# Kernel tuning notes

Measured on AMD Instinct MI355X. Metric: run time of the kernel, lower is better.

Reference implementation:

```python
import jax, jax.numpy as jnp
import numpy as np

CH = 512      # channels
CI = CH // 4  # in_channel = 128
DILS = (1, 4, 8, 12)
GN_GROUPS = 32


def conv2d(x, w, dil=1, pad=0):
    # x: (N,Cin,H,W), w: (Cout,Cin,kh,kw)
    return jax.lax.conv_general_dilated(
        x, w, window_strides=(1, 1), padding=[(pad, pad), (pad, pad)],
        rhs_dilation=(dil, dil),
        dimension_numbers=('NCHW', 'OIHW', 'NCHW'))


def group_norm(x, gamma, beta, groups=GN_GROUPS, eps=1e-5):
    N, C, H, W = x.shape
    xg = x.reshape(N, groups, C // groups, H, W)
    mu = jnp.mean(xg, axis=(2, 3, 4), keepdims=True)
    var = jnp.var(xg, axis=(2, 3, 4), keepdims=True)
    xn = ((xg - mu) * jax.lax.rsqrt(var + eps)).reshape(N, C, H, W)
    return xn * gamma[None, :, None, None] + beta[None, :, None, None]


def dyn_branch(xd, w_cat, d):
    # dynamic filter: (N, 9, H, W), softmax over the K=9 taps per pixel
    f = jax.nn.softmax(conv2d(xd, w_cat, dil=d, pad=d), axis=1)
    N, C, H, W = xd.shape
    xp = jnp.pad(xd, ((0, 0), (0, 0), (d, d), (d, d)))
    # fused unfold + weighted sum: accumulate 9 shifted views * per-pixel weight
    out = jnp.zeros_like(xd)
    k = 0
    for i in range(3):
        for j in range(3):
            out = out + xp[:, :, i * d:i * d + H, j * d:j * d + W] * f[:, k:k + 1]
            k += 1
    return out


def setup_inputs():
    key = jax.random.key(0)
    ks = jax.random.split(key, 16)
    s = 0.05
    return {
        'x': jax.random.normal(ks[0], (4, CH, 128, 128), jnp.float32),
        'w_scale1': jax.random.normal(ks[1], (CI, CH, 1, 1), jnp.float32) * s,
        'gn1_g': jnp.ones((CI,), jnp.float32),
        'gn1_b': jnp.zeros((CI,), jnp.float32),
        'w_cata': jax.random.normal(ks[2], (9, CI, 3, 3), jnp.float32) * s,
        'w_catb': jax.random.normal(ks[3], (9, CI, 3, 3), jnp.float32) * s,
        'w_catc': jax.random.normal(ks[4], (9, CI, 3, 3), jnp.float32) * s,
        'w_catd': jax.random.normal(ks[5], (9, CI, 3, 3), jnp.float32) * s,
        'w_scale2': jax.random.normal(ks[6], (CI, 5 * CI, 1, 1), jnp.float32) * s,
        'gn2_g': jnp.ones((CI,), jnp.float32),
        'gn2_b': jnp.zeros((CI,), jnp.float32),
        'w_scale3': jax.random.normal(ks[7], (CH, CI, 1, 1), jnp.float32) * s,
        'gn3_g': jnp.ones((CH,), jnp.float32),
        'gn3_b': jnp.zeros((CH,), jnp.float32),
    }


def reference(x, w_scale1, gn1_g, gn1_b, w_cata, w_catb, w_catc, w_catd,
              w_scale2, gn2_g, gn2_b, w_scale3, gn3_g, gn3_b):
    # scale1: 1x1 conv -> GN -> ReLU
    xd = jax.nn.relu(group_norm(conv2d(x, w_scale1), gn1_g, gn1_b))
    # four dilated dynamic-filter branches (unfold + softmax-weighted reduce)
    outs = [dyn_branch(xd, w, d)
            for w, d in zip((w_cata, w_catb, w_catc, w_catd), DILS)]
    cat = jnp.concatenate([xd] + outs, axis=1)  # (N, 5*CI, H, W)
    y = jax.nn.relu(group_norm(conv2d(cat, w_scale2), gn2_g, gn2_b))
    y = jax.nn.relu(group_norm(conv2d(y, w_scale3), gn3_g, gn3_b))
    return y
```

## Files before the change

kernel.cpp:

```cpp
#include <hip/hip_runtime.h>
#include <math.h>

#define HW 16384

typedef float f32x4 __attribute__((ext_vector_type(4)));
typedef __bf16 bf16x8 __attribute__((ext_vector_type(8)));
typedef unsigned short u16x4 __attribute__((ext_vector_type(4)));
typedef unsigned short u16x8 __attribute__((ext_vector_type(8)));

__device__ __forceinline__ unsigned short f2bf(float f) {
  unsigned u = __float_as_uint(f);
  u += 0x7fffu + ((u >> 16) & 1u);
  return (unsigned short)(u >> 16);
}
__device__ __forceinline__ float bf2f(unsigned short s) {
  return __uint_as_float(((unsigned)s) << 16);
}

__global__ void prep_kernel(const float* __restrict__ w1, const float* __restrict__ w2,
                            const float* __restrict__ w3,
                            const float* __restrict__ wa, const float* __restrict__ wb,
                            const float* __restrict__ wc, const float* __restrict__ wd,
                            unsigned short* __restrict__ w1b, unsigned short* __restrict__ w2b,
                            unsigned short* __restrict__ w3b, unsigned short* __restrict__ wr) {
  int idx = blockIdx.x * 256 + threadIdx.x;
  if (idx < 65536) { w1b[idx] = f2bf(w1[idx]); }
  else if (idx < 147456) { int j = idx - 65536; w2b[j] = f2bf(w2[j]); }
  else if (idx < 212992) { int j = idx - 147456; w3b[j] = f2bf(w3[j]); }
  else if (idx < 286720) {
    int j = idx - 212992;
    int br = j / 18432, rem = j % 18432;
    int tap = rem / 2048, rem2 = rem % 2048;
    int kt = rem2 / 128, c = rem2 % 128;
    const float* w = (br == 0) ? wa : (br == 1) ? wb : (br == 2) ? wc : wd;
    float v = (kt < 9) ? w[(kt * 128 + c) * 9 + tap] : 0.f;
    wr[j] = f2bf(v);
  }
}

__global__ __launch_bounds__(256) void conv1f_kernel(
    const float* __restrict__ x, const unsigned short* __restrict__ w1b,
    float* __restrict__ out) {
  __shared__ float xs[2][64][65];
  int t = threadIdx.x;
  int wv = t >> 6, lane = t & 63, lr = lane & 15, lg = lane >> 4;
  int n = blockIdx.y;
  int p0 = blockIdx.x * 64;
  const float* xn = x + (size_t)n * 512 * HW + p0;
  f32x4 acc[8];
#pragma unroll
  for (int cb = 0; cb < 8; ++cb) acc[cb] = (f32x4){0.f, 0.f, 0.f, 0.f};

  int ci_l = t >> 4, px4 = (t & 15) * 4;
  float4 r[4];

#pragma unroll
  for (int pass = 0; pass < 4; ++pass)
    r[pass] = *(const float4*)(xn + (size_t)(pass * 16 + ci_l) * HW + px4);
#pragma unroll
  for (int pass = 0; pass < 4; ++pass) {
    int cl = pass * 16 + ci_l;
    xs[0][cl][px4 + 0] = r[pass].x; xs[0][cl][px4 + 1] = r[pass].y;
    xs[0][cl][px4 + 2] = r[pass].z; xs[0][cl][px4 + 3] = r[pass].w;
  }

  for (int kt = 0; kt < 8; ++kt) {
    int cur = kt & 1;
    if (kt < 7) {
#pragma unroll
      for (int pass = 0; pass < 4; ++pass)
        r[pass] = *(const float4*)(xn + (size_t)((kt + 1) * 64 + pass * 16 + ci_l) * HW + px4);
    }
    __syncthreads();
#pragma unroll
    for (int ks = 0; ks < 2; ++ks) {
      bf16x8 a;
#pragma unroll
      for (int j = 0; j < 8; ++j) {
        unsigned short us = f2bf(xs[cur][ks * 32 + lg * 8 + j][wv * 16 + lr]);
        a[j] = *(__bf16*)&us;
      }
#pragma unroll
      for (int cb = 0; cb < 8; ++cb) {
        bf16x8 b = *(const bf16x8*)(w1b + (size_t)(cb * 16 + lr) * 512
                                    + kt * 64 + ks * 32 + lg * 8);
        acc[cb] = __builtin_amdgcn_mfma_f32_16x16x32_bf16(a, b, acc[cb], 0, 0, 0);
      }
    }
    if (kt < 7) {
#pragma unroll
      for (int pass = 0; pass < 4; ++pass) {
        int cl = pass * 16 + ci_l;
        xs[cur ^ 1][cl][px4 + 0] = r[pass].x; xs[cur ^ 1][cl][px4 + 1] = r[pass].y;
        xs[cur ^ 1][cl][px4 + 2] = r[pass].z; xs[cur ^ 1][cl][px4 + 3] = r[pass].w;
      }
    }
  }
  float* on = out + (size_t)n * HW * 128;
#pragma unroll
  for (int cb = 0; cb < 8; ++cb)
#pragma unroll
    for (int r2 = 0; r2 < 4; ++r2)
      on[(size_t)(p0 + wv * 16 + lg * 4 + r2) * 128 + cb * 16 + lr] = acc[cb][r2];
}

template<int K>
__global__ __launch_bounds__(256) void conv_pm_kernel(
    const unsigned short* __restrict__ act, const unsigned short* __restrict__ w,
    float* __restrict__ out) {
  int wv = threadIdx.x >> 6, lane = threadIdx.x & 63;
  int lr = lane & 15, lg = lane >> 4;
  int n = blockIdx.y;
  int p0 = blockIdx.x * 64 + wv * 16;
  const unsigned short* an = act + (size_t)n * HW * K;
  f32x4 acc[8];
#pragma unroll
  for (int cb = 0; cb < 8; ++cb) acc[cb] = (f32x4){0.f, 0.f, 0.f, 0.f};
  const unsigned short* ap = an + (size_t)(p0 + lr) * K + lg * 8;
  const unsigned short* bp = w + (size_t)lr * K + lg * 8;
  for (int ks = 0; ks < K / 32; ++ks) {
    bf16x8 a = *(const bf16x8*)(ap + ks * 32);
#pragma unroll
    for (int cb = 0; cb < 8; ++cb) {
      bf16x8 b = *(const bf16x8*)(bp + (size_t)cb * 16 * K + ks * 32);
      acc[cb] = __builtin_amdgcn_mfma_f32_16x16x32_bf16(a, b, acc[cb], 0, 0, 0);
    }
  }
  float* on = out + (size_t)n * HW * 128;
#pragma unroll
  for (int cb = 0; cb < 8; ++cb)
#pragma unroll
    for (int r = 0; r < 4; ++r)
      on[(size_t)(p0 + lg * 4 + r) * 128 + cb * 16 + lr] = acc[cb][r];
}

__global__ __launch_bounds__(256) void conv3_kernel(
    const unsigned short* __restrict__ y, const unsigned short* __restrict__ w3,
    unsigned short* __restrict__ outb, float* __restrict__ part) {
  int wv = threadIdx.x >> 6, lane = threadIdx.x & 63;
  int lr = lane & 15, lg = lane >> 4;
  int n = blockIdx.y, zc = blockIdx.z;
  int co0 = zc * 128 + wv * 32;
  int p0 = blockIdx.x * 128;
  const unsigned short* yn = y + (size_t)n * HW * 128;
  f32x4 acc[2][8];
#pragma unroll
  for (int pr = 0; pr < 2; ++pr)
#pragma unroll
    for (int cb = 0; cb < 8; ++cb) acc[pr][cb] = (f32x4){0.f, 0.f, 0.f, 0.f};
#pragma unroll
  for (int ks = 0; ks < 4; ++ks) {
    bf16x8 a0 = *(const bf16x8*)(w3 + (size_t)(co0 + lr) * 128 + ks * 32 + lg * 8);
    bf16x8 a1 = *(const bf16x8*)(w3 + (size_t)(co0 + 16 + lr) * 128 + ks * 32 + lg * 8);
#pragma unroll
    for (int cb = 0; cb < 8; ++cb) {
      bf16x8 b = *(const bf16x8*)(yn + (size_t)(p0 + cb * 16 + lr) * 128 + ks * 32 + lg * 8);
      acc[0][cb] = __builtin_amdgcn_mfma_f32_16x16x32_bf16(a0, b, acc[0][cb], 0, 0, 0);
      acc[1][cb] = __builtin_amdgcn_mfma_f32_16x16x32_bf16(a1, b, acc[1][cb], 0, 0, 0);
    }
  }
  unsigned short* on = outb + (size_t)n * 512 * HW;
  float s[2] = {0.f, 0.f}, ss[2] = {0.f, 0.f};
#pragma unroll
  for (int pr = 0; pr < 2; ++pr)
#pragma unroll
    for (int cb = 0; cb < 8; ++cb)
#pragma unroll
      for (int r = 0; r < 4; ++r) {
        float v = acc[pr][cb][r];
        on[(size_t)(co0 + pr * 16 + lg * 4 + r) * HW + p0 + cb * 16 + lr] = f2bf(v);
        s[pr] += v; ss[pr] += v * v;
      }
#pragma unroll
  for (int pr = 0; pr < 2; ++pr) {
    float a = s[pr], b = ss[pr];
    for (int m = 1; m < 64; m <<= 1) { a += __shfl_xor(a, m); b += __shfl_xor(b, m); }
    if (lane == 0) {
      float* pp = part + ((((size_t)n * 4 + zc) * 128 + blockIdx.x) * 8 + wv * 2 + pr) * 2;
      pp[0] = a; pp[1] = b;
    }
  }
}

__global__ void gnf3_kernel(const float* __restrict__ part, float* __restrict__ stats) {
  int t = threadIdx.x;
  int n = t >> 5, g = t & 31;
  int zc = g >> 3, sub = g & 7;
  float s = 0.f, ss = 0.f;
  for (int xb = 0; xb < 128; ++xb) {
    const float* pp = part + ((((size_t)n * 4 + zc) * 128 + xb) * 8 + sub) * 2;
    s += pp[0]; ss += pp[1];
  }
  float inv = 1.f / (16.f * HW);
  float mean = s * inv, var = ss * inv - mean * mean;
  stats[2 * t] = mean; stats[2 * t + 1] = rsqrtf(var + 1e-5f);
}

__global__ __launch_bounds__(256) void gn3_apply_kernel(
    const unsigned short* __restrict__ y3b, const float* __restrict__ stats,
    const float* __restrict__ gamma, const float* __restrict__ beta,
    float* __restrict__ out) {
  size_t e8 = ((size_t)blockIdx.x * 256 + threadIdx.x) * 8;
  int n = (int)(e8 >> 23);
  int c = (int)((e8 >> 14) & 511);
  int sg = n * 32 + (c >> 4);
  float mean = stats[2 * sg], rstd = stats[2 * sg + 1];
  float scale = rstd * gamma[c];
  float shift = beta[c] - mean * scale;
  u16x8 u = *(const u16x8*)(y3b + e8);
  float4 o0, o1;
  o0.x = fmaxf(fmaf(bf2f(u[0]), scale, shift), 0.f);
  o0.y = fmaxf(fmaf(bf2f(u[1]), scale, shift), 0.f);
  o0.z = fmaxf(fmaf(bf2f(u[2]), scale, shift), 0.f);
  o0.w = fmaxf(fmaf(bf2f(u[3]), scale, shift), 0.f);
  o1.x = fmaxf(fmaf(bf2f(u[4]), scale, shift), 0.f);
  o1.y = fmaxf(fmaf(bf2f(u[5]), scale, shift), 0.f);
  o1.z = fmaxf(fmaf(bf2f(u[6]), scale, shift), 0.f);
  o1.w = fmaxf(fmaf(bf2f(u[7]), scale, shift), 0.f);
  *(float4*)(out + e8) = o0;
  *(float4*)(out + e8 + 4) = o1;
}

__global__ __launch_bounds__(256) void gnp_pm_kernel(const float* __restrict__ src,
                                                     float* __restrict__ part) {
  int t = threadIdx.x;
  int g = t & 31, ph = t >> 5;
  int pt = blockIdx.x, n = blockIdx.y;
  const float* b = src + (size_t)n * HW * 128 + 4 * g;
  float s = 0.f, ss = 0.f;
  for (int p = pt * 256 + ph; p < (pt + 1) * 256; p += 8) {
    float4 v = *(const float4*)(b + (size_t)p * 128);
    s += v.x + v.y + v.z + v.w;
    ss += v.x * v.x + v.y * v.y + v.z * v.z + v.w * v.w;
  }
  __shared__ float sh[256], sh2[256];
  sh[t] = s; sh2[t] = ss; __syncthreads();
  if (t < 128) { sh[t] += sh[t + 128]; sh2[t] += sh2[t + 128]; } __syncthreads();
  if (t < 64)  { sh[t] += sh[t + 64];  sh2[t] += sh2[t + 64];  } __syncthreads();
  if (t < 32) {
    float a = sh[t] + sh[t + 32], b2 = sh2[t] + sh2[t + 32];
    float* pp = part + ((size_t)(n * 64 + pt) * 32 + t) * 2;
    pp[0] = a; pp[1] = b2;
  }
}

__global__ void gnf_pm_kernel(const float* __restrict__ part, float* __restrict__ stats) {
  int t = threadIdx.x;
  int n = t >> 5, g = t & 31;
  float s = 0.f, ss = 0.f;
  for (int pt = 0; pt < 64; ++pt) {
    const float* pp = part + ((size_t)(n * 64 + pt) * 32 + g) * 2;
    s += pp[0]; ss += pp[1];
  }
  float inv = 1.f / (4.f * HW);
  float mean = s * inv, var = ss * inv - mean * mean;
  stats[2 * t] = mean; stats[2 * t + 1] = rsqrtf(var + 1e-5f);
}

__global__ __launch_bounds__(256) void gna_pm_kernel(
    const float* __restrict__ src, const float* __restrict__ stats,
    const float* __restrict__ gamma, const float* __restrict__ beta,
    unsigned short* __restrict__ dst, int ldd) {
  int idx = blockIdx.x * 256 + threadIdx.x;
  int g = idx & 31;
  int p = (idx >> 5) & (HW - 1);
  int n = idx >> 19;
  float4 v = *(const float4*)(src + ((size_t)n * HW + p) * 128 + 4 * g);
  int sg = n * 32 + g;
  float mean = stats[2 * sg], rstd = stats[2 * sg + 1];
  float sc0 = rstd * gamma[4 * g + 0], sc1 = rstd * gamma[4 * g + 1];
  float sc2 = rstd * gamma[4 * g + 2], sc3 = rstd * gamma[4 * g + 3];
  float sh0 = beta[4 * g + 0] - mean * sc0, sh1 = beta[4 * g + 1] - mean * sc1;
  float sh2 = beta[4 * g + 2] - mean * sc2, sh3 = beta[4 * g + 3] - mean * sc3;
  u16x4 o;
  o[0] = f2bf(fmaxf(fmaf(v.x, sc0, sh0), 0.f));
  o[1] = f2bf(fmaxf(fmaf(v.y, sc1, sh1), 0.f));
  o[2] = f2bf(fmaxf(fmaf(v.z, sc2, sh2), 0.f));
  o[3] = f2bf(fmaxf(fmaf(v.w, sc3, sh3), 0.f));
  *(u16x4*)(dst + ((size_t)n * HW + p) * ldd + 4 * g) = o;
}

#define DP 136

__global__ __launch_bounds__(512, 4) void dynfused6_kernel(
    const unsigned short* __restrict__ cat, const unsigned short* __restrict__ wr,
    unsigned short* __restrict__ catw) {
  extern __shared__ char smem[];
  unsigned short* rowbuf = (unsigned short*)smem;
  float* fl = (float*)(smem + 3 * 88 * DP * 2);
  int t = threadIdx.x;
  int bid = blockIdx.x;
  int rh = ((bid & 7) << 5) + (bid >> 3);
  int row = rh >> 1, hw = rh & 1;
  int n = blockIdx.y >> 2, br = blockIdx.y & 3;
  int d = (br == 0) ? 1 : 4 * br;
  const unsigned short* xb = cat + (size_t)n * HW * 640;

  int rg[3] = { max(row - d, 0), row, min(row + d, 127) };
  bool rv[3] = { row - d >= 0, true, row + d < 128 };
  int cbase = hw * 64 - 12;

  {
    u16x8 vreg[9];
#pragma unroll
    for (int k = 0; k < 9; ++k) {
      int ci = t + (k << 9);
      if (k == 8 && ci >= 4224) continue;
      int s = (ci >= 2816) ? 2 : (ci >= 1408 ? 1 : 0);
      int rem = ci - s * 1408;
      int slot = rem >> 4, c = rem & 15;
      int gcol = min(max(cbase + slot, 0), 127);
      vreg[k] = *(const u16x8*)(xb + ((size_t)(rg[s] * 128 + gcol)) * 640 + c * 8);
    }
#pragma unroll
    for (int k = 0; k < 9; ++k) {
      int ci = t + (k << 9);
      if (k == 8 && ci >= 4224) continue;
      int s = (ci >= 2816) ? 2 : (ci >= 1408 ? 1 : 0);
      int rem = ci - s * 1408;
      int slot = rem >> 4, c = rem & 15;
      *(u16x8*)(rowbuf + ((size_t)s * 88 + slot) * DP + c * 8) = vreg[k];
    }
  }
  __syncthreads();

  if (t < 256) {
    int wv = t >> 6, lane = t & 63;
    int lr = lane & 15, lg = lane >> 4;
    const unsigned short* wb = wr + (size_t)br * 9 * 16 * 128;
    const bf16x8 zb = {(__bf16)0.f, (__bf16)0.f, (__bf16)0.f, (__bf16)0.f,
                       (__bf16)0.f, (__bf16)0.f, (__bf16)0.f, (__bf16)0.f};
    f32x4 acc = (f32x4){0.f, 0.f, 0.f, 0.f};
    int pxl = wv * 16 + lr;
    int gw = hw * 64 + pxl;
#pragma unroll
    for (int tap = 0; tap < 9; ++tap) {
      int s = tap / 3;
      int dw = (tap % 3 - 1) * d;
      int slot = 12 + pxl + dw;
      bool val = rv[s] && ((unsigned)(gw + dw) < 128u);
      const unsigned short* ap = rowbuf + ((size_t)s * 88 + slot) * DP + lg * 8;
      const unsigned short* wt = wb + (size_t)(tap * 16 + lr) * 128 + lg * 8;
#pragma unroll
      for (int ks = 0; ks < 4; ++ks) {
        bf16x8 a = *(const bf16x8*)(ap + ks * 32);
        if (!val) a = zb;
        bf16x8 b = *(const bf16x8*)(wt + ks * 32);
        acc = __builtin_amdgcn_mfma_f32_16x16x32_bf16(a, b, acc, 0, 0, 0);
      }
    }
#pragma unroll
    for (int r = 0; r < 4; ++r) {
      float v = acc[r];
      float m = (lr < 9) ? v : -3.0e38f;
#pragma unroll
      for (int msk = 1; msk < 16; msk <<= 1) m = fmaxf(m, __shfl_xor(m, msk));
      float e = (lr < 9) ? expf(v - m) : 0.f;
      float su = e;
#pragma unroll
      for (int msk = 1; msk < 16; msk <<= 1) su += __shfl_xor(su, msk);
      fl[(wv * 16 + lg * 4 + r) * 17 + lr] = e / su;
    }
  }
  __syncthreads();

  {
    int pxl = t >> 3, c8 = t & 7;
    int gw = hw * 64 + pxl;
    float oacc[16];
#pragma unroll
    for (int i = 0; i < 16; ++i) oacc[i] = 0.f;
#pragma unroll
    for (int tap = 0; tap < 9; ++tap) {
      int s = tap / 3;
      int dw = (tap % 3 - 1) * d;
      int slot = 12 + pxl + dw;
      bool val = rv[s] && ((unsigned)(gw + dw) < 128u);
      float f = val ? fl[pxl * 17 + tap] : 0.f;
      const unsigned short* ap = rowbuf + ((size_t)s * 88 + slot) * DP + c8 * 16;
#pragma unroll
      for (int cc = 0; cc < 2; ++cc) {
        u16x8 u = *(const u16x8*)(ap + cc * 8);
#pragma unroll
        for (int i = 0; i < 8; ++i)
          oacc[cc * 8 + i] = fmaf(f, bf2f(u[i]), oacc[cc * 8 + i]);
      }
    }
    unsigned short* orow = catw + ((size_t)n * HW + row * 128 + gw) * 640
                           + 128 * (br + 1) + c8 * 16;
#pragma unroll
    for (int cc = 0; cc < 2; ++cc) {
      u16x8 o;
#pragma unroll
      for (int i = 0; i < 8; ++i) o[i] = f2bf(oacc[cc * 8 + i]);
      *(u16x8*)(orow + cc * 8) = o;
    }
  }
}

extern "C" void kernel_launch(void* const* d_in, const int* in_sizes, int n_in,
                              void* d_out, int out_size, void* d_ws, size_t ws_size,
                              hipStream_t stream) {
  const float* x   = (const float*)d_in[0];
  const float* w1  = (const float*)d_in[1];
  const float* g1  = (const float*)d_in[2];
  const float* b1  = (const float*)d_in[3];
  const float* wca = (const float*)d_in[4];
  const float* wcb = (const float*)d_in[5];
  const float* wcc = (const float*)d_in[6];
  const float* wcd = (const float*)d_in[7];
  const float* w2  = (const float*)d_in[8];
  const float* g2  = (const float*)d_in[9];
  const float* b2  = (const float*)d_in[10];
  const float* w3  = (const float*)d_in[11];
  const float* g3  = (const float*)d_in[12];
  const float* b3  = (const float*)d_in[13];
  float* out = (float*)d_out;

  float* ws = (float*)d_ws;
  float* xd_t = ws + 16777216;
  unsigned short* cat = (unsigned short*)(ws + 25165824);
  float* y2t = ws;
  unsigned short* y2b = (unsigned short*)(ws + 8388608);
  unsigned short* y3b = (unsigned short*)(ws + 25165824);
  float* aux = ws + 46137344;
  unsigned short* w1b = (unsigned short*)(aux);
  unsigned short* w2b = (unsigned short*)(aux + 32768);
  unsigned short* w3b = (unsigned short*)(aux + 73728);
  unsigned short* wr  = (unsigned short*)(aux + 106496);
  float* part  = aux + 143360;
  float* part3 = aux + 159744;
  float* st1   = aux + 192512;
  float* st2   = aux + 192768;
  float* st3   = aux + 193024;

  dim3 blk(256);
  const int dynLds = 3 * 88 * DP * 2 + 64 * 17 * 4;
  (void)hipFuncSetAttribute((const void*)dynfused6_kernel,
                            hipFuncAttributeMaxDynamicSharedMemorySize, dynLds);

  prep_kernel<<<dim3(1120), blk, 0, stream>>>(w1, w2, w3, wca, wcb, wcc, wcd,
                                              w1b, w2b, w3b, wr);

  conv1f_kernel<<<dim3(256, 4), blk, 0, stream>>>(x, w1b, xd_t);
  gnp_pm_kernel<<<dim3(64, 4), blk, 0, stream>>>(xd_t, part);
  gnf_pm_kernel<<<dim3(1), dim3(128), 0, stream>>>(part, st1);
  gna_pm_kernel<<<dim3(8192), blk, 0, stream>>>(xd_t, st1, g1, b1, cat, 640);

  dynfused6_kernel<<<dim3(256, 16), dim3(512), dynLds, stream>>>(cat, wr, cat);

  conv_pm_kernel<640><<<dim3(256, 4), blk, 0, stream>>>(cat, w2b, y2t);
  gnp_pm_kernel<<<dim3(64, 4), blk, 0, stream>>>(y2t, part);
  gnf_pm_kernel<<<dim3(1), dim3(128), 0, stream>>>(part, st2);
  gna_pm_kernel<<<dim3(8192), blk, 0, stream>>>(y2t, st2, g2, b2, y2b, 128);

  conv3_kernel<<<dim3(128, 4, 4), blk, 0, stream>>>(y2b, w3b, y3b, part3);
  gnf3_kernel<<<dim3(1), dim3(128), 0, stream>>>(part3, st3);
  gn3_apply_kernel<<<dim3(16384), blk, 0, stream>>>(y3b, st3, g3, b3, out);
}
```

Before: 385.2 us.

## Fuse GroupNorm partial stats into conv epilogues and store bf16 intermediates

The conv1 and conv2 kernels now compute per-block GroupNorm sum and sum-of-squares partials in their epilogues using wave shuffles and shared memory. This removes the separate stats pass that re-read the fp32 outputs. The conv outputs are written directly as bf16, into the concatenated buffer for conv1, and normalized in place by a new apply kernel. This cuts fp32 intermediate traffic and one launch per GroupNorm stage. The trade-off is that statistics are taken on pre-rounding fp32 values while the normalization is applied to bf16-rounded values, plus a longer serial final reduction over 256 partials.

```diff
diff --git a/kernel.cpp b/kernel.cpp
--- a/kernel.cpp
+++ b/kernel.cpp
@@ -38,10 +38,41 @@
   }
 }
 
+__device__ __forceinline__ void gn_partial_epilogue(
+    f32x4 (&acc)[8], int wv, int lane, int t, int n, int blkx,
+    float* __restrict__ part, float (*ps)[32], float (*pss)[32]) {
+  float gs[8], gss[8];
+#pragma unroll
+  for (int cb = 0; cb < 8; ++cb) {
+    float s = 0.f, ss = 0.f;
+#pragma unroll
+    for (int r = 0; r < 4; ++r) { float v = acc[cb][r]; s += v; ss += v * v; }
+#pragma unroll
+    for (int m = 0; m < 4; ++m) {
+      const int msk[4] = {1, 2, 16, 32};
+      s += __shfl_xor(s, msk[m]); ss += __shfl_xor(ss, msk[m]);
+    }
+    gs[cb] = s; gss[cb] = ss;
+  }
+  if (lane < 16 && (lane & 3) == 0) {
+    int q = lane >> 2;
+#pragma unroll
+    for (int cb = 0; cb < 8; ++cb) { ps[wv][cb * 4 + q] = gs[cb]; pss[wv][cb * 4 + q] = gss[cb]; }
+  }
+  __syncthreads();
+  if (t < 32) {
+    float a = ps[0][t] + ps[1][t] + ps[2][t] + ps[3][t];
+    float b = pss[0][t] + pss[1][t] + pss[2][t] + pss[3][t];
+    float* pp = part + ((size_t)(n * 32 + t) * 256 + blkx) * 2;
+    pp[0] = a; pp[1] = b;
+  }
+}
+
 __global__ __launch_bounds__(256) void conv1f_kernel(
     const float* __restrict__ x, const unsigned short* __restrict__ w1b,
-    float* __restrict__ out) {
+    unsigned short* __restrict__ outb, float* __restrict__ part) {
   __shared__ float xs[2][64][65];
+  __shared__ float ps[4][32], pss[4][32];
   int t = threadIdx.x;
   int wv = t >> 6, lane = t & 63, lr = lane & 15, lg = lane >> 4;
   int n = blockIdx.y;
@@ -96,19 +127,23 @@
       }
     }
   }
-  float* on = out + (size_t)n * HW * 128;
+  unsigned short* on = outb + (size_t)n * HW * 640;
 #pragma unroll
   for (int cb = 0; cb < 8; ++cb)
 #pragma unroll
     for (int r2 = 0; r2 < 4; ++r2)
-      on[(size_t)(p0 + wv * 16 + lg * 4 + r2) * 128 + cb * 16 + lr] = acc[cb][r2];
+      on[(size_t)(p0 + wv * 16 + lg * 4 + r2) * 640 + cb * 16 + lr] = f2bf(acc[cb][r2]);
+  __syncthreads();
+  gn_partial_epilogue(acc, wv, lane, t, n, blockIdx.x, part, ps, pss);
 }
 
 template<int K>
 __global__ __launch_bounds__(256) void conv_pm_kernel(
     const unsigned short* __restrict__ act, const unsigned short* __restrict__ w,
-    float* __restrict__ out) {
-  int wv = threadIdx.x >> 6, lane = threadIdx.x & 63;
+    unsigned short* __restrict__ outb, float* __restrict__ part, int ldd) {
+  __shared__ float ps[4][32], pss[4][32];
+  int t = threadIdx.x;
+  int wv = t >> 6, lane = t & 63;
   int lr = lane & 15, lg = lane >> 4;
   int n = blockIdx.y;
   int p0 = blockIdx.x * 64 + wv * 16;
@@ -126,12 +161,48 @@
       acc[cb] = __builtin_amdgcn_mfma_f32_16x16x32_bf16(a, b, acc[cb], 0, 0, 0);
     }
   }
-  float* on = out + (size_t)n * HW * 128;
+  unsigned short* on = outb + (size_t)n * HW * ldd;
 #pragma unroll
   for (int cb = 0; cb < 8; ++cb)
 #pragma unroll
     for (int r = 0; r < 4; ++r)
-      on[(size_t)(p0 + lg * 4 + r) * 128 + cb * 16 + lr] = acc[cb][r];
+      on[(size_t)(p0 + lg * 4 + r) * ldd + cb * 16 + lr] = f2bf(acc[cb][r]);
+  gn_partial_epilogue(acc, wv, lane, t, n, blockIdx.x, part, ps, pss);
+}
+
+__global__ void gnf256_kernel(const float* __restrict__ part, float* __restrict__ stats) {
+  int t = threadIdx.x;
+  float s = 0.f, ss = 0.f;
+  for (int b = 0; b < 256; ++b) {
+    const float* pp = part + ((size_t)t * 256 + b) * 2;
+    s += pp[0]; ss += pp[1];
+  }
+  float inv = 1.f / (4.f * HW);
+  float mean = s * inv, var = ss * inv - mean * mean;
+  stats[2 * t] = mean; stats[2 * t + 1] = rsqrtf(var + 1e-5f);
+}
+
+__global__ __launch_bounds__(256) void gna_ip_kernel(
+    unsigned short* __restrict__ dst, const float* __restrict__ stats,
+    const float* __restrict__ gamma, const float* __restrict__ beta, int ldd) {
+  int idx = blockIdx.x * 256 + threadIdx.x;
+  int g = idx & 31;
+  int p = (idx >> 5) & (HW - 1);
+  int n = idx >> 19;
+  unsigned short* ptr = dst + ((size_t)n * HW + p) * ldd + 4 * g;
+  u16x4 v = *(u16x4*)ptr;
+  int sg = n * 32 + g;
+  float mean = stats[2 * sg], rstd = stats[2 * sg + 1];
+  float sc0 = rstd * gamma[4 * g + 0], sc1 = rstd * gamma[4 * g + 1];
+  float sc2 = rstd * gamma[4 * g + 2], sc3 = rstd * gamma[4 * g + 3];
+  float sh0 = beta[4 * g + 0] - mean * sc0, sh1 = beta[4 * g + 1] - mean * sc1;
+  float sh2 = beta[4 * g + 2] - mean * sc2, sh3 = beta[4 * g + 3] - mean * sc3;
+  u16x4 o;
+  o[0] = f2bf(fmaxf(fmaf(bf2f(v[0]), sc0, sh0), 0.f));
+  o[1] = f2bf(fmaxf(fmaf(bf2f(v[1]), sc1, sh1), 0.f));
+  o[2] = f2bf(fmaxf(fmaf(bf2f(v[2]), sc2, sh2), 0.f));
+  o[3] = f2bf(fmaxf(fmaf(bf2f(v[3]), sc3, sh3), 0.f));
+  *(u16x4*)ptr = o;
 }
 
 __global__ __launch_bounds__(256) void conv3_kernel(
@@ -221,65 +292,6 @@
   *(float4*)(out + e8 + 4) = o1;
 }
 
-__global__ __launch_bounds__(256) void gnp_pm_kernel(const float* __restrict__ src,
-                                                     float* __restrict__ part) {
-  int t = threadIdx.x;
-  int g = t & 31, ph = t >> 5;
-  int pt = blockIdx.x, n = blockIdx.y;
-  const float* b = src + (size_t)n * HW * 128 + 4 * g;
-  float s = 0.f, ss = 0.f;
-  for (int p = pt * 256 + ph; p < (pt + 1) * 256; p += 8) {
-    float4 v = *(const float4*)(b + (size_t)p * 128);
-    s += v.x + v.y + v.z + v.w;
-    ss += v.x * v.x + v.y * v.y + v.z * v.z + v.w * v.w;
-  }
-  __shared__ float sh[256], sh2[256];
-  sh[t] = s; sh2[t] = ss; __syncthreads();
-  if (t < 128) { sh[t] += sh[t + 128]; sh2[t] += sh2[t + 128]; } __syncthreads();
-  if (t < 64)  { sh[t] += sh[t + 64];  sh2[t] += sh2[t + 64];  } __syncthreads();
-  if (t < 32) {
-    float a = sh[t] + sh[t + 32], b2 = sh2[t] + sh2[t + 32];
-    float* pp = part + ((size_t)(n * 64 + pt) * 32 + t) * 2;
-    pp[0] = a; pp[1] = b2;
-  }
-}
-
-__global__ void gnf_pm_kernel(const float* __restrict__ part, float* __restrict__ stats) {
-  int t = threadIdx.x;
-  int n = t >> 5, g = t & 31;
-  float s = 0.f, ss = 0.f;
-  for (int pt = 0; pt < 64; ++pt) {
-    const float* pp = part + ((size_t)(n * 64 + pt) * 32 + g) * 2;
-    s += pp[0]; ss += pp[1];
-  }
-  float inv = 1.f / (4.f * HW);
-  float mean = s * inv, var = ss * inv - mean * mean;
-  stats[2 * t] = mean; stats[2 * t + 1] = rsqrtf(var + 1e-5f);
-}
-
-__global__ __launch_bounds__(256) void gna_pm_kernel(
-    const float* __restrict__ src, const float* __restrict__ stats,
-    const float* __restrict__ gamma, const float* __restrict__ beta,
-    unsigned short* __restrict__ dst, int ldd) {
-  int idx = blockIdx.x * 256 + threadIdx.x;
-  int g = idx & 31;
-  int p = (idx >> 5) & (HW - 1);
-  int n = idx >> 19;
-  float4 v = *(const float4*)(src + ((size_t)n * HW + p) * 128 + 4 * g);
-  int sg = n * 32 + g;
-  float mean = stats[2 * sg], rstd = stats[2 * sg + 1];
-  float sc0 = rstd * gamma[4 * g + 0], sc1 = rstd * gamma[4 * g + 1];
-  float sc2 = rstd * gamma[4 * g + 2], sc3 = rstd * gamma[4 * g + 3];
-  float sh0 = beta[4 * g + 0] - mean * sc0, sh1 = beta[4 * g + 1] - mean * sc1;
-  float sh2 = beta[4 * g + 2] - mean * sc2, sh3 = beta[4 * g + 3] - mean * sc3;
-  u16x4 o;
-  o[0] = f2bf(fmaxf(fmaf(v.x, sc0, sh0), 0.f));
-  o[1] = f2bf(fmaxf(fmaf(v.y, sc1, sh1), 0.f));
-  o[2] = f2bf(fmaxf(fmaf(v.z, sc2, sh2), 0.f));
-  o[3] = f2bf(fmaxf(fmaf(v.w, sc3, sh3), 0.f));
-  *(u16x4*)(dst + ((size_t)n * HW + p) * ldd + 4 * g) = o;
-}
-
 #define DP 136
 
 __global__ __launch_bounds__(512, 4) void dynfused6_kernel(
@@ -418,9 +430,7 @@
   float* out = (float*)d_out;
 
   float* ws = (float*)d_ws;
-  float* xd_t = ws + 16777216;
   unsigned short* cat = (unsigned short*)(ws + 25165824);
-  float* y2t = ws;
   unsigned short* y2b = (unsigned short*)(ws + 8388608);
   unsigned short* y3b = (unsigned short*)(ws + 25165824);
   float* aux = ws + 46137344;
@@ -429,10 +439,10 @@
   unsigned short* w3b = (unsigned short*)(aux + 73728);
   unsigned short* wr  = (unsigned short*)(aux + 106496);
   float* part  = aux + 143360;
-  float* part3 = aux + 159744;
-  float* st1   = aux + 192512;
-  float* st2   = aux + 192768;
-  float* st3   = aux + 193024;
+  float* part3 = aux + 208896;
+  float* st1   = aux + 241664;
+  float* st2   = aux + 241920;
+  float* st3   = aux + 242176;
 
   dim3 blk(256);
   const int dynLds = 3 * 88 * DP * 2 + 64 * 17 * 4;
@@ -442,17 +452,15 @@
   prep_kernel<<<dim3(1120), blk, 0, stream>>>(w1, w2, w3, wca, wcb, wcc, wcd,
                                               w1b, w2b, w3b, wr);
 
-  conv1f_kernel<<<dim3(256, 4), blk, 0, stream>>>(x, w1b, xd_t);
-  gnp_pm_kernel<<<dim3(64, 4), blk, 0, stream>>>(xd_t, part);
-  gnf_pm_kernel<<<dim3(1), dim3(128), 0, stream>>>(part, st1);
-  gna_pm_kernel<<<dim3(8192), blk, 0, stream>>>(xd_t, st1, g1, b1, cat, 640);
+  conv1f_kernel<<<dim3(256, 4), blk, 0, stream>>>(x, w1b, cat, part);
+  gnf256_kernel<<<dim3(1), dim3(128), 0, stream>>>(part, st1);
+  gna_ip_kernel<<<dim3(8192), blk, 0, stream>>>(cat, st1, g1, b1, 640);
 
   dynfused6_kernel<<<dim3(256, 16), dim3(512), dynLds, stream>>>(cat, wr, cat);
 
-  conv_pm_kernel<640><<<dim3(256, 4), blk, 0, stream>>>(cat, w2b, y2t);
-  gnp_pm_kernel<<<dim3(64, 4), blk, 0, stream>>>(y2t, part);
-  gnf_pm_kernel<<<dim3(1), dim3(128), 0, stream>>>(part, st2);
-  gna_pm_kernel<<<dim3(8192), blk, 0, stream>>>(y2t, st2, g2, b2, y2b, 128);
+  conv_pm_kernel<640><<<dim3(256, 4), blk, 0, stream>>>(cat, w2b, y2b, part, 128);
+  gnf256_kernel<<<dim3(1), dim3(128), 0, stream>>>(part, st2);
+  gna_ip_kernel<<<dim3(8192), blk, 0, stream>>>(y2b, st2, g2, b2, 128);
 
   conv3_kernel<<<dim3(128, 4, 4), blk, 0, stream>>>(y2b, w3b, y3b, part3);
   gnf3_kernel<<<dim3(1), dim3(128), 0, stream>>>(part3, st3);
```

Result: faster. 372.7 us (-3.2%).
